# Kernel tuning notes

Measured on AMD Instinct MI355X. Metric: run time of the kernel, lower is better.

## Reference

```python
import jax, jax.numpy as jnp
import numpy as np

B, S, N, D, H, C, E, DG = 2, 512, 20000, 384, 3, 128, 320000, 128
NEG_SLOPE = 0.2  # PyG GATConv default


def setup_inputs() -> dict:
    key = jax.random.key(0)
    ks = jax.random.split(key, 10)
    p = lambda k, sh: jax.random.normal(k, sh, jnp.float32) * 0.02
    return dict(
        x_enc=jax.random.normal(ks[0], (B, S, D), jnp.float32),
        mask=jax.random.uniform(ks[1], (B, N), dtype=jnp.float32),
        edge_index=jax.random.randint(ks[2], (2, E), 0, N),
        Wq=p(ks[3], (N, S)), bq=jnp.zeros((N,), jnp.float32),
        Wm=p(ks[4], (D, 1)), bm=jnp.zeros((D,), jnp.float32),
        Wlin=p(ks[5], (H * C, D)),
        att_src=p(ks[6], (H, C)), att_dst=p(ks[7], (H, C)),
        bias_gat=jnp.zeros((H * C,), jnp.float32),
        Wproj=p(ks[8], (S, N)), bproj=jnp.zeros((S,), jnp.float32),
        Wtemp=p(ks[9], (DG, H * C)), btemp=jnp.zeros((DG,), jnp.float32),
    )


def reference(x_enc, mask, edge_index, Wq, bq, Wm, bm, Wlin, att_src, att_dst,
              bias_gat, Wproj, bproj, Wtemp, btemp):
    # q = query_proj(x_enc.permute(0,2,1)).permute(0,2,1)  -> [B, N, D]
    q = jnp.einsum('bsd,ns->bnd', x_enc, Wq) + bq[None, :, None]
    # mask_proj: Linear(1, D) on mask[..., None]  -> [B, N, D]
    mask_embed = mask[..., None] * Wm[:, 0] + bm
    x = (q + mask_embed).reshape(B * N, D)

    # batch edge_index with per-graph node offsets, then add self-loops (PyG default)
    offs = (jnp.arange(B, dtype=edge_index.dtype) * N)[:, None]
    src = (edge_index[0][None, :] + offs).reshape(-1)
    dst = (edge_index[1][None, :] + offs).reshape(-1)
    loops = jnp.arange(B * N, dtype=edge_index.dtype)
    src = jnp.concatenate([src, loops])
    dst = jnp.concatenate([dst, loops])

    # GATConv: shared linear, per-head attention
    xp = (x @ Wlin.T).reshape(B * N, H, C)                  # [BN, H, C]
    a_src = jnp.einsum('nhc,hc->nh', xp, att_src)           # [BN, H]
    a_dst = jnp.einsum('nhc,hc->nh', xp, att_dst)
    e = jax.nn.leaky_relu(a_src[src] + a_dst[dst], NEG_SLOPE)  # [Etot, H]
    # segment-softmax over incoming edges of each destination node
    emax = jax.ops.segment_max(e, dst, num_segments=B * N)
    ee = jnp.exp(e - emax[dst])
    denom = jax.ops.segment_sum(ee, dst, num_segments=B * N)
    alpha = ee / denom[dst]                                  # [Etot, H]
    out = jax.ops.segment_sum(xp[src] * alpha[..., None], dst, num_segments=B * N)
    out = out.reshape(B, N, H * C) + bias_gat                # concat heads + bias

    # dropout is identity in eval
    # project: Linear(N, S) over node dim -> [B, S, H*C]
    out = jnp.einsum('bnf,sn->bsf', out, Wproj) + bproj[None, :, None]
    # temp_project: Linear(H*C, d_graph)
    out = out @ Wtemp.T + btemp
    return out
```

## Files before the change

### kernel.cpp

```cpp
#include <hip/hip_runtime.h>
#include <hip/hip_bf16.h>
#include <cstdint>

#define B_   2
#define S_   512
#define N_   20000
#define H_   3
#define C_   128
#define E_   320000
#define DG_  128
#define D_   384
#define BN_  (B_ * N_)
#define F_   (H_ * C_)
#define ECSR_ (E_ + N_)

#define MPADQ 20096
#define MPADL 40064

#define PNS2 32
#define PCH2 640

using short8  = __attribute__((ext_vector_type(8))) short;
using floatx4 = __attribute__((ext_vector_type(4))) float;

__device__ __forceinline__ float b2f(unsigned short u) {
  union { unsigned int i; float f; } x; x.i = ((unsigned int)u) << 16; return x.f;
}
__device__ __forceinline__ unsigned short f2b(float f) {
  __hip_bfloat16 b = __float2bfloat16(f);
  return *reinterpret_cast<unsigned short*>(&b);
}

struct bf4 { __hip_bfloat16 a, b, c, d; };

#define NWQ4 ((MPADQ * 512) / 4)
#define NXE4 ((B_ * S_ * D_) / 4)
#define NWL4 ((F_ * D_) / 4)
#define NWP4 ((S_ * N_) / 4)
#define NWT4 ((DG_ * F_) / 4)
#define NCV0 NWQ4
#define NCV1 (NCV0 + NXE4)
#define NCV2 (NCV1 + NWL4)
#define NCV3 (NCV2 + NWP4)
#define NCV4 (NCV3 + NWT4)
#define NCVTOT (NCV4 + (F_ + DG_) * 64)

__device__ __forceinline__ void cv4(const float* __restrict__ src,
                                    __hip_bfloat16* __restrict__ dst, int e) {
  float4 v = *(const float4*)(src + e);
  bf4 r{__float2bfloat16(v.x), __float2bfloat16(v.y),
        __float2bfloat16(v.z), __float2bfloat16(v.w)};
  *(bf4*)(dst + e) = r;
}

__global__ __launch_bounds__(256) void conv_all_kernel(
    const float* __restrict__ Wq,    __hip_bfloat16* __restrict__ WqB,
    const float* __restrict__ xe,    __hip_bfloat16* __restrict__ xeB,
    const float* __restrict__ Wlin,  __hip_bfloat16* __restrict__ WlinB,
    const float* __restrict__ Wproj, __hip_bfloat16* __restrict__ WprojB,
    const float* __restrict__ Wtemp, __hip_bfloat16* __restrict__ WtempB,
    const float* __restrict__ Wm,    const float* __restrict__ bm,
    float* __restrict__ epi,         float* __restrict__ swt) {
  int idx = blockIdx.x * 256 + threadIdx.x;
  if (idx < NCV0) {
    int e = idx * 4;
    int row = e >> 9;
    float4 v = make_float4(0.f, 0.f, 0.f, 0.f);
    if (row < N_) v = *(const float4*)(Wq + e);
    bf4 r{__float2bfloat16(v.x), __float2bfloat16(v.y),
          __float2bfloat16(v.z), __float2bfloat16(v.w)};
    *(bf4*)(WqB + e) = r;
  } else if (idx < NCV1) {
    cv4(xe, xeB, (idx - NCV0) * 4);
  } else if (idx < NCV2) {
    cv4(Wlin, WlinB, (idx - NCV1) * 4);
  } else if (idx < NCV3) {
    cv4(Wproj, WprojB, (idx - NCV2) * 4);
  } else if (idx < NCV4) {
    cv4(Wtemp, WtempB, (idx - NCV3) * 4);
  } else {
    int w = (idx - NCV4) >> 6;
    int lane = idx & 63;
    if (w < F_) {
      float s0 = 0.f, s1 = 0.f, s2 = 0.f;
      const float* row = Wlin + (size_t)w * D_;
      for (int d = lane; d < D_; d += 64) {
        float wv = row[d];
        s0 += wv; s1 += Wm[d] * wv; s2 += bm[d] * wv;
      }
#pragma unroll
      for (int o = 32; o > 0; o >>= 1) {
        s0 += __shfl_down(s0, o); s1 += __shfl_down(s1, o); s2 += __shfl_down(s2, o);
      }
      if (lane == 0) { epi[w] = s0; epi[F_ + w] = s1; epi[2 * F_ + w] = s2; }
    } else {
      int g = w - F_;
      float s = 0.f;
      const float* row = Wtemp + (size_t)g * F_;
      for (int f = lane; f < F_; f += 64) s += row[f];
#pragma unroll
      for (int o = 32; o > 0; o >>= 1) s += __shfl_down(s, o);
      if (lane == 0) swt[g] = s;
    }
  }
}

template <int EPI>
__global__ __launch_bounds__(256) void mfma_gemm_nt(
    const __hip_bfloat16* __restrict__ A, const __hip_bfloat16* __restrict__ Bt,
    __hip_bfloat16* __restrict__ Cout, int K, int Mvalid, int ldc,
    size_t bstrideB, size_t bstrideC,
    const float* __restrict__ bq, const float* __restrict__ mask,
    const float* __restrict__ epi) {
  const int tid = threadIdx.x;
  const int m0 = blockIdx.x * 128;
  const int n0 = blockIdx.y * 128;
  const int bz = blockIdx.z;

  const unsigned short* Ap = (const unsigned short*)A;
  const unsigned short* Bp = (const unsigned short*)(Bt + bstrideB * bz);

  __shared__ __align__(16) unsigned short As[128][40];
  __shared__ __align__(16) unsigned short Bs[128][40];

  const int wave = tid >> 6, lane = tid & 63;
  const int wm = (wave & 1) * 64, wn = (wave >> 1) * 64;
  const int lrow = lane & 15, lk = (lane >> 4) * 8;

  const int srow = tid >> 2;
  const int skoff = (tid & 3) * 8;

  floatx4 acc[4][4];
#pragma unroll
  for (int i = 0; i < 4; ++i)
#pragma unroll
    for (int j = 0; j < 4; ++j) acc[i][j] = floatx4{0.f, 0.f, 0.f, 0.f};

  for (int k0 = 0; k0 < K; k0 += 32) {
    int4 av0 = *(const int4*)(Ap + (size_t)(m0 + srow) * K + k0 + skoff);
    int4 av1 = *(const int4*)(Ap + (size_t)(m0 + 64 + srow) * K + k0 + skoff);
    int4 bv0 = *(const int4*)(Bp + (size_t)(n0 + srow) * K + k0 + skoff);
    int4 bv1 = *(const int4*)(Bp + (size_t)(n0 + 64 + srow) * K + k0 + skoff);
    __syncthreads();
    *(int4*)&As[srow][skoff] = av0;
    *(int4*)&As[64 + srow][skoff] = av1;
    *(int4*)&Bs[srow][skoff] = bv0;
    *(int4*)&Bs[64 + srow][skoff] = bv1;
    __syncthreads();
    short8 af[4], bf[4];
#pragma unroll
    for (int mt = 0; mt < 4; ++mt)
      af[mt] = *(const short8*)&As[wm + mt * 16 + lrow][lk];
#pragma unroll
    for (int nt = 0; nt < 4; ++nt)
      bf[nt] = *(const short8*)&Bs[wn + nt * 16 + lrow][lk];
#pragma unroll
    for (int mt = 0; mt < 4; ++mt)
#pragma unroll
      for (int nt = 0; nt < 4; ++nt)
        acc[mt][nt] = __builtin_amdgcn_mfma_f32_16x16x32_bf16(af[mt], bf[nt],
                                                              acc[mt][nt], 0, 0, 0);
  }

  __hip_bfloat16* Cb = Cout + bstrideC * bz;
#pragma unroll
  for (int mt = 0; mt < 4; ++mt) {
#pragma unroll
    for (int r = 0; r < 4; ++r) {
      int rg = m0 + wm + mt * 16 + (lane >> 4) * 4 + r;
      if (rg < Mvalid) {
        float bqv = 0.f, mkv = 0.f;
        if (EPI) {
          bqv = bq[rg];
          mkv = mask[bz * N_ + rg];
        }
#pragma unroll
        for (int nt = 0; nt < 4; ++nt) {
          int cg = n0 + wn + nt * 16 + lrow;
          float v = acc[mt][nt][r];
          if (EPI) v += bqv * epi[cg] + mkv * epi[F_ + cg] + epi[2 * F_ + cg];
          Cb[(size_t)rg * ldc + cg] = __float2bfloat16(v);
        }
      }
    }
  }
}

__global__ __launch_bounds__(256) void gemm_gn(
    const __hip_bfloat16* __restrict__ A, const __hip_bfloat16* __restrict__ Bt,
    __hip_bfloat16* __restrict__ gnT) {
  const int tid = threadIdx.x;
  const int m0 = blockIdx.x * 128;

  const unsigned short* Ap = (const unsigned short*)A;
  const unsigned short* Bp = (const unsigned short*)Bt;

  __shared__ __align__(16) unsigned short As[128][40];
  __shared__ __align__(16) unsigned short Bs[128][40];

  const int wave = tid >> 6, lane = tid & 63;
  const int wm = (wave & 1) * 64, wn = (wave >> 1) * 64;
  const int lrow = lane & 15, lk = (lane >> 4) * 8;
  const int srow = tid >> 2;
  const int skoff = (tid & 3) * 8;

  floatx4 acc[4][4];
#pragma unroll
  for (int i = 0; i < 4; ++i)
#pragma unroll
    for (int j = 0; j < 4; ++j) acc[i][j] = floatx4{0.f, 0.f, 0.f, 0.f};

  for (int k0 = 0; k0 < F_; k0 += 32) {
    int4 av0 = *(const int4*)(Ap + (size_t)(m0 + srow) * F_ + k0 + skoff);
    int4 av1 = *(const int4*)(Ap + (size_t)(m0 + 64 + srow) * F_ + k0 + skoff);
    int4 bv0 = *(const int4*)(Bp + (size_t)(srow) * F_ + k0 + skoff);
    int4 bv1 = *(const int4*)(Bp + (size_t)(64 + srow) * F_ + k0 + skoff);
    __syncthreads();
    *(int4*)&As[srow][skoff] = av0;
    *(int4*)&As[64 + srow][skoff] = av1;
    *(int4*)&Bs[srow][skoff] = bv0;
    *(int4*)&Bs[64 + srow][skoff] = bv1;
    __syncthreads();
    short8 af[4], bf[4];
#pragma unroll
    for (int mt = 0; mt < 4; ++mt)
      af[mt] = *(const short8*)&As[wm + mt * 16 + lrow][lk];
#pragma unroll
    for (int nt = 0; nt < 4; ++nt)
      bf[nt] = *(const short8*)&Bs[wn + nt * 16 + lrow][lk];
#pragma unroll
    for (int mt = 0; mt < 4; ++mt)
#pragma unroll
      for (int nt = 0; nt < 4; ++nt)
        acc[mt][nt] = __builtin_amdgcn_mfma_f32_16x16x32_bf16(af[mt], bf[nt],
                                                              acc[mt][nt], 0, 0, 0);
  }

#pragma unroll
  for (int mt = 0; mt < 4; ++mt) {
    int rg0 = m0 + wm + mt * 16 + (lane >> 4) * 4;
    if (rg0 < BN_) {
      int b = (rg0 >= N_) ? 1 : 0;
      int n = rg0 - b * N_;
#pragma unroll
      for (int nt = 0; nt < 4; ++nt) {
        int cg = wn + nt * 16 + lrow;
        ushort4 o;
        o.x = f2b(acc[mt][nt][0]); o.y = f2b(acc[mt][nt][1]);
        o.z = f2b(acc[mt][nt][2]); o.w = f2b(acc[mt][nt][3]);
        *(ushort4*)((unsigned short*)gnT + (size_t)b * DG_ * N_ + (size_t)cg * N_ + n) = o;
      }
    }
  }
}

__global__ __launch_bounds__(256) void gemm_proj2(
    const __hip_bfloat16* __restrict__ A, const __hip_bfloat16* __restrict__ Bt,
    float* __restrict__ Ppart) {
  const int tid = threadIdx.x;
  const int m0 = blockIdx.x * 128;
  const int bz = blockIdx.z;
  const int b = bz / PNS2, ks = bz - b * PNS2;
  const int kbeg = ks * PCH2;
  const int kend = (kbeg + PCH2 < N_) ? (kbeg + PCH2) : N_;

  const unsigned short* Ap = (const unsigned short*)A;
  const unsigned short* Bp = (const unsigned short*)(Bt + (size_t)b * DG_ * N_);

  __shared__ __align__(16) unsigned short As[128][40];
  __shared__ __align__(16) unsigned short Bs[128][40];

  const int wave = tid >> 6, lane = tid & 63;
  const int wm = (wave & 1) * 64, wn = (wave >> 1) * 64;
  const int lrow = lane & 15, lk = (lane >> 4) * 8;
  const int srow = tid >> 2;
  const int skoff = (tid & 3) * 8;

  floatx4 acc[4][4];
#pragma unroll
  for (int i = 0; i < 4; ++i)
#pragma unroll
    for (int j = 0; j < 4; ++j) acc[i][j] = floatx4{0.f, 0.f, 0.f, 0.f};

  for (int k0 = kbeg; k0 < kend; k0 += 32) {
    int4 av0 = *(const int4*)(Ap + (size_t)(m0 + srow) * N_ + k0 + skoff);
    int4 av1 = *(const int4*)(Ap + (size_t)(m0 + 64 + srow) * N_ + k0 + skoff);
    int4 bv0 = *(const int4*)(Bp + (size_t)(srow) * N_ + k0 + skoff);
    int4 bv1 = *(const int4*)(Bp + (size_t)(64 + srow) * N_ + k0 + skoff);
    __syncthreads();
    *(int4*)&As[srow][skoff] = av0;
    *(int4*)&As[64 + srow][skoff] = av1;
    *(int4*)&Bs[srow][skoff] = bv0;
    *(int4*)&Bs[64 + srow][skoff] = bv1;
    __syncthreads();
    short8 af[4], bf[4];
#pragma unroll
    for (int mt = 0; mt < 4; ++mt)
      af[mt] = *(const short8*)&As[wm + mt * 16 + lrow][lk];
#pragma unroll
    for (int nt = 0; nt < 4; ++nt)
      bf[nt] = *(const short8*)&Bs[wn + nt * 16 + lrow][lk];
#pragma unroll
    for (int mt = 0; mt < 4; ++mt)
#pragma unroll
      for (int nt = 0; nt < 4; ++nt)
        acc[mt][nt] = __builtin_amdgcn_mfma_f32_16x16x32_bf16(af[mt], bf[nt],
                                                              acc[mt][nt], 0, 0, 0);
  }

  float* Pp = Ppart + (size_t)bz * S_ * DG_;
#pragma unroll
  for (int mt = 0; mt < 4; ++mt) {
#pragma unroll
    for (int r = 0; r < 4; ++r) {
      int rg = m0 + wm + mt * 16 + (lane >> 4) * 4 + r;
#pragma unroll
      for (int nt = 0; nt < 4; ++nt) {
        int cg = wn + nt * 16 + lrow;
        Pp[(size_t)rg * DG_ + cg] = acc[mt][nt][r];
      }
    }
  }
}

__global__ __launch_bounds__(256) void att_kernel(
    const __hip_bfloat16* __restrict__ xp, const float* __restrict__ att_src,
    const float* __restrict__ att_dst, float* __restrict__ a_src,
    float* __restrict__ a_dst) {
  int gid = blockIdx.x * blockDim.x + threadIdx.x;
  int wid = gid >> 6;
  int lane = threadIdx.x & 63;
  if (wid >= BN_ * H_) return;
  int i = wid / H_, h = wid - i * H_;
  const __hip_bfloat16* row = xp + (size_t)i * F_ + h * C_;
  const float* as = att_src + h * C_;
  const float* ad = att_dst + h * C_;
  float v0 = __bfloat162float(row[lane]), v1 = __bfloat162float(row[lane + 64]);
  float s1 = v0 * as[lane] + v1 * as[lane + 64];
  float s2 = v0 * ad[lane] + v1 * ad[lane + 64];
#pragma unroll
  for (int off = 32; off > 0; off >>= 1) {
    s1 += __shfl_down(s1, off);
    s2 += __shfl_down(s2, off);
  }
  if (lane == 0) {
    a_src[i * H_ + h] = s1;
    a_dst[i * H_ + h] = s2;
  }
}

__global__ __launch_bounds__(256) void count_kernel(const int* __restrict__ ei,
                                                    int* __restrict__ counts,
                                                    int* __restrict__ rank) {
  int idx = blockIdx.x * blockDim.x + threadIdx.x;
  if (idx >= E_) return;
  int d = ei[E_ + idx];
  rank[idx] = atomicAdd(&counts[d], 1);
}

__global__ __launch_bounds__(1024) void scan_kernel(const int* __restrict__ counts,
                                                    int* __restrict__ offs) {
  __shared__ int wsum[16];
  __shared__ int carry;
  int t = threadIdx.x, wave = t >> 6, lane = t & 63;
  if (t == 0) carry = 0;
  __syncthreads();
  for (int base = 0; base < N_; base += 1024) {
    int i = base + t;
    int v = (i < N_) ? (counts[i] + 1) : 0;
    int x = v;
#pragma unroll
    for (int o = 1; o < 64; o <<= 1) {
      int y = __shfl_up(x, o);
      if (lane >= o) x += y;
    }
    if (lane == 63) wsum[wave] = x;
    __syncthreads();
    int c = carry;
    if (wave == 0) {
      int w = (lane < 16) ? wsum[lane] : 0;
#pragma unroll
      for (int o = 1; o < 16; o <<= 1) {
        int y = __shfl_up(w, o);
        if (lane >= o) w += y;
      }
      if (lane < 16) wsum[lane] = w;
    }
    __syncthreads();
    int woff = (wave == 0) ? 0 : wsum[wave - 1];
    int excl = c + woff + x - v;
    if (i < N_) offs[i] = excl;
    int total = wsum[15];
    __syncthreads();
    if (t == 0) carry = c + total;
  }
}

__global__ __launch_bounds__(256) void fill_kernel(
    const int* __restrict__ ei, const int* __restrict__ rank,
    const int* __restrict__ offs, const int* __restrict__ counts,
    int* __restrict__ col) {
  int idx = blockIdx.x * blockDim.x + threadIdx.x;
  if (idx >= ECSR_) return;
  if (idx < E_) {
    int sg = ei[idx];
    int dg = ei[E_ + idx];
    col[offs[dg] + rank[idx]] = sg;
  } else {
    int n = idx - E_;
    col[offs[n] + counts[n]] = n;
  }
}

__global__ __launch_bounds__(192) void agg_kernel(
    const int* __restrict__ offs, const int* __restrict__ counts,
    const int* __restrict__ col, const float* __restrict__ a_src,
    const float* __restrict__ a_dst, const __hip_bfloat16* __restrict__ xp,
    const float* __restrict__ bias_gat, __hip_bfloat16* __restrict__ out) {
  int n = blockIdx.x;
  int t = threadIdx.x;
  int q = (t >= 96) ? 1 : 0;
  int tt = t - q * 96;
  int qn = q * N_;
  int i = qn + n;
  int beg = offs[n];
  int nE = counts[n] + 1;
  int h = tt >> 5;

  const ushort4* xp4 = (const ushort4*)xp;
  float ad = a_dst[(size_t)i * 3 + h];
  float ax = 0.f, ay = 0.f, az = 0.f, aw = 0.f, sw = 0.f;

  int j = 0;
  for (; j + 4 <= nE; j += 4) {
    int s0 = col[beg + j + 0] + qn;
    int s1 = col[beg + j + 1] + qn;
    int s2 = col[beg + j + 2] + qn;
    int s3 = col[beg + j + 3] + qn;
    float e0 = a_src[(size_t)s0 * 3 + h] + ad;
    float e1 = a_src[(size_t)s1 * 3 + h] + ad;
    float e2 = a_src[(size_t)s2 * 3 + h] + ad;
    float e3 = a_src[(size_t)s3 * 3 + h] + ad;
    e0 = (e0 > 0.f) ? e0 : 0.2f * e0;
    e1 = (e1 > 0.f) ? e1 : 0.2f * e1;
    e2 = (e2 > 0.f) ? e2 : 0.2f * e2;
    e3 = (e3 > 0.f) ? e3 : 0.2f * e3;
    float w0 = __expf(e0), w1 = __expf(e1);
    float w2 = __expf(e2), w3 = __expf(e3);
    sw += (w0 + w1) + (w2 + w3);
    ushort4 v0 = xp4[(size_t)s0 * 96 + tt];
    ushort4 v1 = xp4[(size_t)s1 * 96 + tt];
    ushort4 v2 = xp4[(size_t)s2 * 96 + tt];
    ushort4 v3 = xp4[(size_t)s3 * 96 + tt];
    ax = fmaf(w0, b2f(v0.x), ax); ay = fmaf(w0, b2f(v0.y), ay);
    az = fmaf(w0, b2f(v0.z), az); aw = fmaf(w0, b2f(v0.w), aw);
    ax = fmaf(w1, b2f(v1.x), ax); ay = fmaf(w1, b2f(v1.y), ay);
    az = fmaf(w1, b2f(v1.z), az); aw = fmaf(w1, b2f(v1.w), aw);
    ax = fmaf(w2, b2f(v2.x), ax); ay = fmaf(w2, b2f(v2.y), ay);
    az = fmaf(w2, b2f(v2.z), az); aw = fmaf(w2, b2f(v2.w), aw);
    ax = fmaf(w3, b2f(v3.x), ax); ay = fmaf(w3, b2f(v3.y), ay);
    az = fmaf(w3, b2f(v3.z), az); aw = fmaf(w3, b2f(v3.w), aw);
  }
  for (; j < nE; ++j) {
    int s0 = col[beg + j] + qn;
    float e0 = a_src[(size_t)s0 * 3 + h] + ad;
    e0 = (e0 > 0.f) ? e0 : 0.2f * e0;
    float w0 = __expf(e0);
    sw += w0;
    ushort4 v0 = xp4[(size_t)s0 * 96 + tt];
    ax = fmaf(w0, b2f(v0.x), ax); ay = fmaf(w0, b2f(v0.y), ay);
    az = fmaf(w0, b2f(v0.z), az); aw = fmaf(w0, b2f(v0.w), aw);
  }

  float r = 1.0f / sw;
  const float4 bg = *(const float4*)(bias_gat + tt * 4);
  ushort4 o;
  o.x = f2b(ax * r + bg.x);
  o.y = f2b(ay * r + bg.y);
  o.z = f2b(az * r + bg.z);
  o.w = f2b(aw * r + bg.w);
  *(ushort4*)((unsigned short*)out + (size_t)i * F_ + tt * 4) = o;
}

__global__ __launch_bounds__(128) void final_kernel(
    const float* __restrict__ Ppart, const float* __restrict__ bproj,
    const float* __restrict__ swt, const float* __restrict__ btemp,
    float* __restrict__ out) {
  int bs = blockIdx.x;
  int b = bs >> 9;
  int s = bs & (S_ - 1);
  int g = threadIdx.x;
  float acc = btemp[g] + bproj[s] * swt[g];
  const float* pp = Ppart + ((size_t)b * PNS2 * S_ + s) * DG_ + g;
  for (int ns = 0; ns < PNS2; ++ns) acc += pp[(size_t)ns * S_ * DG_];
  out[(size_t)bs * DG_ + g] = acc;
}

extern "C" void kernel_launch(void* const* d_in, const int* in_sizes, int n_in,
                              void* d_out, int out_size, void* d_ws, size_t ws_size,
                              hipStream_t stream) {
  const float* x_enc   = (const float*)d_in[0];
  const float* mask    = (const float*)d_in[1];
  const int*   ei      = (const int*)d_in[2];
  const float* Wq      = (const float*)d_in[3];
  const float* bq      = (const float*)d_in[4];
  const float* Wm      = (const float*)d_in[5];
  const float* bm      = (const float*)d_in[6];
  const float* Wlin    = (const float*)d_in[7];
  const float* att_src = (const float*)d_in[8];
  const float* att_dst = (const float*)d_in[9];
  const float* bias_gat= (const float*)d_in[10];
  const float* Wproj   = (const float*)d_in[11];
  const float* bproj   = (const float*)d_in[12];
  const float* Wtemp   = (const float*)d_in[13];
  const float* btemp   = (const float*)d_in[14];
  float* outp = (float*)d_out;

  char* ws = (char*)d_ws;
  size_t off = 0;
  auto alloc = [&](size_t bytes) {
    char* p = ws + off;
    off = (off + bytes + 255) & ~(size_t)255;
    return p;
  };

  const size_t GNT_OFF = (size_t)B_ * PNS2 * S_ * DG_ * 4;
  char* regionA = alloc(GNT_OFF + (size_t)B_ * DG_ * N_ * 2);
  __hip_bfloat16* Wq_b = (__hip_bfloat16*)regionA;
  float* Ppart = (float*)regionA;
  __hip_bfloat16* gnT  = (__hip_bfloat16*)(regionA + GNT_OFF);

  __hip_bfloat16* xeB    = (__hip_bfloat16*)alloc((size_t)B_ * S_ * D_ * 2);
  __hip_bfloat16* yT     = (__hip_bfloat16*)alloc((size_t)B_ * F_ * S_ * 2);
  __hip_bfloat16* xp     = (__hip_bfloat16*)alloc((size_t)BN_ * F_ * 2);
  __hip_bfloat16* gat    = (__hip_bfloat16*)alloc((size_t)MPADL * F_ * 2);
  __hip_bfloat16* WlinB  = (__hip_bfloat16*)alloc((size_t)F_ * D_ * 2);
  __hip_bfloat16* WprojB = (__hip_bfloat16*)alloc((size_t)S_ * N_ * 2);
  __hip_bfloat16* WtempB = (__hip_bfloat16*)alloc((size_t)DG_ * F_ * 2);
  float* epi   = (float*)alloc((size_t)3 * F_ * 4);
  float* swt   = (float*)alloc((size_t)DG_ * 4);
  float* a_src = (float*)alloc((size_t)BN_ * H_ * 4);
  float* a_dst = (float*)alloc((size_t)BN_ * H_ * 4);
  int* counts  = (int*)alloc((size_t)N_ * 4);
  int* offsb   = (int*)alloc((size_t)N_ * 4);
  int* rank    = (int*)alloc((size_t)E_ * 4);
  int* col     = (int*)alloc((size_t)ECSR_ * 4);
  if (off > ws_size) return;

  hipMemsetAsync(counts, 0, (size_t)N_ * 4, stream);
  hipMemsetAsync(gat + (size_t)BN_ * F_, 0, (size_t)(MPADL - BN_) * F_ * 2, stream);

  count_kernel<<<(E_ + 255) / 256, 256, 0, stream>>>(ei, counts, rank);
  scan_kernel<<<1, 1024, 0, stream>>>(counts, offsb);
  fill_kernel<<<(ECSR_ + 255) / 256, 256, 0, stream>>>(ei, rank, offsb, counts, col);

  conv_all_kernel<<<NCVTOT / 256, 256, 0, stream>>>(
      Wq, Wq_b, x_enc, xeB, Wlin, WlinB, Wproj, WprojB, Wtemp, WtempB,
      Wm, bm, epi, swt);

  mfma_gemm_nt<0><<<dim3(F_ / 128, S_ / 128, B_), 256, 0, stream>>>(
      WlinB, xeB, yT, D_, F_, S_, (size_t)S_ * D_, (size_t)F_ * S_,
      nullptr, nullptr, nullptr);
  mfma_gemm_nt<1><<<dim3(MPADQ / 128, F_ / 128, B_), 256, 0, stream>>>(
      Wq_b, yT, xp, S_, N_, F_, (size_t)F_ * S_, (size_t)N_ * F_,
      bq, mask, epi);

  att_kernel<<<(BN_ * H_ + 3) / 4, 256, 0, stream>>>(xp, att_src, att_dst, a_src, a_dst);
  agg_kernel<<<N_, 192, 0, stream>>>(offsb, counts, col, a_src, a_dst,
                                     xp, bias_gat, gat);

  gemm_gn<<<dim3(MPADL / 128, 1, 1), 256, 0, stream>>>(gat, WtempB, gnT);
  gemm_proj2<<<dim3(S_ / 128, 1, B_ * PNS2), 256, 0, stream>>>(WprojB, gnT, Ppart);
  final_kernel<<<B_ * S_, 128, 0, stream>>>(Ppart, bproj, swt, btemp, outp);
}
```

Measured before the change: 374.6 us.

## Parallelize CSR offset scan across blocks and split aggregation per batch

Replaces the single-block serial prefix scan over node degrees with a three-kernel multi-block scan (per-block scan, scan of block totals, add-back), so the CSR build no longer runs on one workgroup. The aggregation kernel now launches one block per (batch, node) instead of covering both batches in one 192-thread block. Those blocks have 128 threads, of which 32 exit immediately, so a third of the lanes are wasted. The change adds two extra kernel launches in exchange for more parallel scan work.

Result: faster. 354.8 us (-5.3%).

```diff
diff --git a/kernel.cpp b/kernel.cpp
--- a/kernel.cpp
+++ b/kernel.cpp
@@ -358,42 +358,54 @@
   rank[idx] = atomicAdd(&counts[d], 1);
 }
 
-__global__ __launch_bounds__(1024) void scan_kernel(const int* __restrict__ counts,
-                                                    int* __restrict__ offs) {
+#define SCB 1024
+#define NSCB ((N_ + SCB - 1) / SCB)
+__global__ __launch_bounds__(1024) void scan1_kernel(const int* __restrict__ counts,
+                                                     int* __restrict__ offs,
+                                                     int* __restrict__ btot) {
   __shared__ int wsum[16];
-  __shared__ int carry;
   int t = threadIdx.x, wave = t >> 6, lane = t & 63;
-  if (t == 0) carry = 0;
+  int i = blockIdx.x * SCB + t;
+  int v = (i < N_) ? (counts[i] + 1) : 0;
+  int x = v;
+#pragma unroll
+  for (int o = 1; o < 64; o <<= 1) {
+    int y = __shfl_up(x, o);
+    if (lane >= o) x += y;
+  }
+  if (lane == 63) wsum[wave] = x;
   __syncthreads();
-  for (int base = 0; base < N_; base += 1024) {
-    int i = base + t;
-    int v = (i < N_) ? (counts[i] + 1) : 0;
-    int x = v;
-#pragma unroll
-    for (int o = 1; o < 64; o <<= 1) {
-      int y = __shfl_up(x, o);
-      if (lane >= o) x += y;
+  if (wave == 0) {
+    int w = (lane < 16) ? wsum[lane] : 0;
+#pragma unroll
+    for (int o = 1; o < 16; o <<= 1) {
+      int y = __shfl_up(w, o);
+      if (lane >= o) w += y;
     }
-    if (lane == 63) wsum[wave] = x;
-    __syncthreads();
-    int c = carry;
-    if (wave == 0) {
-      int w = (lane < 16) ? wsum[lane] : 0;
-#pragma unroll
-      for (int o = 1; o < 16; o <<= 1) {
-        int y = __shfl_up(w, o);
-        if (lane >= o) w += y;
-      }
-      if (lane < 16) wsum[lane] = w;
-    }
-    __syncthreads();
-    int woff = (wave == 0) ? 0 : wsum[wave - 1];
-    int excl = c + woff + x - v;
-    if (i < N_) offs[i] = excl;
-    int total = wsum[15];
-    __syncthreads();
-    if (t == 0) carry = c + total;
-  }
+    if (lane < 16) wsum[lane] = w;
+  }
+  __syncthreads();
+  int woff = (wave == 0) ? 0 : wsum[wave - 1];
+  if (i < N_) offs[i] = woff + x - v;
+  if (t == 0) btot[blockIdx.x] = wsum[15];
+}
+
+__global__ __launch_bounds__(64) void scan2_kernel(int* __restrict__ btot) {
+  int lane = threadIdx.x;
+  int v = (lane < NSCB) ? btot[lane] : 0;
+  int x = v;
+#pragma unroll
+  for (int o = 1; o < 64; o <<= 1) {
+    int y = __shfl_up(x, o);
+    if (lane >= o) x += y;
+  }
+  if (lane < NSCB) btot[lane] = x - v;
+}
+
+__global__ __launch_bounds__(256) void scan3_kernel(int* __restrict__ offs,
+                                                    const int* __restrict__ btot) {
+  int i = blockIdx.x * 256 + threadIdx.x;
+  if (i < N_) offs[i] += btot[i >> 10];
 }
 
 __global__ __launch_bounds__(256) void fill_kernel(
@@ -412,20 +424,21 @@
   }
 }
 
-__global__ __launch_bounds__(192) void agg_kernel(
+__global__ __launch_bounds__(128) void agg_kernel(
     const int* __restrict__ offs, const int* __restrict__ counts,
     const int* __restrict__ col, const float* __restrict__ a_src,
     const float* __restrict__ a_dst, const __hip_bfloat16* __restrict__ xp,
     const float* __restrict__ bias_gat, __hip_bfloat16* __restrict__ out) {
-  int n = blockIdx.x;
-  int t = threadIdx.x;
-  int q = (t >= 96) ? 1 : 0;
-  int tt = t - q * 96;
+  int bi = blockIdx.x;
+  int q = (bi >= N_) ? 1 : 0;
+  int n = bi - q * N_;
   int qn = q * N_;
   int i = qn + n;
+  int t = threadIdx.x;
+  if (t >= 96) return;
   int beg = offs[n];
   int nE = counts[n] + 1;
-  int h = tt >> 5;
+  int h = t >> 5;
 
   const ushort4* xp4 = (const ushort4*)xp;
   float ad = a_dst[(size_t)i * 3 + h];
@@ -448,10 +461,10 @@
     float w0 = __expf(e0), w1 = __expf(e1);
     float w2 = __expf(e2), w3 = __expf(e3);
     sw += (w0 + w1) + (w2 + w3);
-    ushort4 v0 = xp4[(size_t)s0 * 96 + tt];
-    ushort4 v1 = xp4[(size_t)s1 * 96 + tt];
-    ushort4 v2 = xp4[(size_t)s2 * 96 + tt];
-    ushort4 v3 = xp4[(size_t)s3 * 96 + tt];
+    ushort4 v0 = xp4[(size_t)s0 * 96 + t];
+    ushort4 v1 = xp4[(size_t)s1 * 96 + t];
+    ushort4 v2 = xp4[(size_t)s2 * 96 + t];
+    ushort4 v3 = xp4[(size_t)s3 * 96 + t];
     ax = fmaf(w0, b2f(v0.x), ax); ay = fmaf(w0, b2f(v0.y), ay);
     az = fmaf(w0, b2f(v0.z), az); aw = fmaf(w0, b2f(v0.w), aw);
     ax = fmaf(w1, b2f(v1.x), ax); ay = fmaf(w1, b2f(v1.y), ay);
@@ -467,19 +480,19 @@
     e0 = (e0 > 0.f) ? e0 : 0.2f * e0;
     float w0 = __expf(e0);
     sw += w0;
-    ushort4 v0 = xp4[(size_t)s0 * 96 + tt];
+    ushort4 v0 = xp4[(size_t)s0 * 96 + t];
     ax = fmaf(w0, b2f(v0.x), ax); ay = fmaf(w0, b2f(v0.y), ay);
     az = fmaf(w0, b2f(v0.z), az); aw = fmaf(w0, b2f(v0.w), aw);
   }
 
   float r = 1.0f / sw;
-  const float4 bg = *(const float4*)(bias_gat + tt * 4);
+  const float4 bg = *(const float4*)(bias_gat + t * 4);
   ushort4 o;
   o.x = f2b(ax * r + bg.x);
   o.y = f2b(ay * r + bg.y);
   o.z = f2b(az * r + bg.z);
   o.w = f2b(aw * r + bg.w);
-  *(ushort4*)((unsigned short*)out + (size_t)i * F_ + tt * 4) = o;
+  *(ushort4*)((unsigned short*)out + (size_t)i * F_ + t * 4) = o;
 }
 
 __global__ __launch_bounds__(128) void final_kernel(
@@ -545,13 +558,16 @@
   int* offsb   = (int*)alloc((size_t)N_ * 4);
   int* rank    = (int*)alloc((size_t)E_ * 4);
   int* col     = (int*)alloc((size_t)ECSR_ * 4);
+  int* btot    = (int*)alloc((size_t)NSCB * 4);
   if (off > ws_size) return;
 
   hipMemsetAsync(counts, 0, (size_t)N_ * 4, stream);
   hipMemsetAsync(gat + (size_t)BN_ * F_, 0, (size_t)(MPADL - BN_) * F_ * 2, stream);
 
   count_kernel<<<(E_ + 255) / 256, 256, 0, stream>>>(ei, counts, rank);
-  scan_kernel<<<1, 1024, 0, stream>>>(counts, offsb);
+  scan1_kernel<<<NSCB, SCB, 0, stream>>>(counts, offsb, btot);
+  scan2_kernel<<<1, 64, 0, stream>>>(btot);
+  scan3_kernel<<<(N_ + 255) / 256, 256, 0, stream>>>(offsb, btot);
   fill_kernel<<<(ECSR_ + 255) / 256, 256, 0, stream>>>(ei, rank, offsb, counts, col);
 
   conv_all_kernel<<<NCVTOT / 256, 256, 0, stream>>>(
@@ -566,8 +582,8 @@
       bq, mask, epi);
 
   att_kernel<<<(BN_ * H_ + 3) / 4, 256, 0, stream>>>(xp, att_src, att_dst, a_src, a_dst);
-  agg_kernel<<<N_, 192, 0, stream>>>(offsb, counts, col, a_src, a_dst,
-                                     xp, bias_gat, gat);
+  agg_kernel<<<BN_, 128, 0, stream>>>(offsb, counts, col, a_src, a_dst,
+                                      xp, bias_gat, gat);
 
   gemm_gn<<<dim3(MPADL / 128, 1, 1), 256, 0, stream>>>(gat, WtempB, gnT);
   gemm_proj2<<<dim3(S_ / 128, 1, B_ * PNS2), 256, 0, stream>>>(WprojB, gnT, Ppart);
```
